# Kernel tuning notes

Measured on AMD Instinct MI355X. Metric: run time of the kernel, lower is better.

The kernel has to match this reference:

```python
import jax, jax.numpy as jnp
import numpy as np

WINDOW_SIZE = 11
SIGMA = 1.5
CHANNEL = 3
L = 2.0
C1 = (0.01 * L) ** 2
C2 = (0.03 * L) ** 2
WEIGHTS = jnp.asarray([0.0448, 0.2856, 0.3001, 0.2363, 0.1333], dtype=jnp.float32)


def _create_window(window_size=WINDOW_SIZE, channel=CHANNEL):
    x = jnp.arange(window_size, dtype=jnp.float32)
    g = jnp.exp(-((x - window_size // 2) ** 2) / (2.0 * SIGMA ** 2))
    g = g / g.sum()
    w2d = jnp.outer(g, g)  # (ws, ws)
    # depthwise kernel, OIHW with I=1, O=channel
    return jnp.broadcast_to(w2d[None, None], (channel, 1, window_size, window_size))


def _depthwise_conv(x, w):
    # x: (B,C,H,W), w: (C,1,kh,kw), groups=C, VALID padding
    return jax.lax.conv_general_dilated(
        x, w, window_strides=(1, 1), padding='VALID',
        feature_group_count=x.shape[1],
        dimension_numbers=('NCHW', 'OIHW', 'NCHW'))


def _ssim_level(img1, img2, window):
    mu1 = _depthwise_conv(img1, window)
    mu2 = _depthwise_conv(img2, window)
    mu1_sq = mu1 * mu1
    mu2_sq = mu2 * mu2
    mu1_mu2 = mu1 * mu2
    sigma1_sq = _depthwise_conv(img1 * img1, window) - mu1_sq
    sigma2_sq = _depthwise_conv(img2 * img2, window) - mu2_sq
    sigma12 = _depthwise_conv(img1 * img2, window) - mu1_mu2
    v1 = 2.0 * sigma12 + C2
    v2 = sigma1_sq + sigma2_sq + C2
    cs = jnp.mean(v1 / v2)
    ssim_map = (2.0 * mu1_mu2 + C1) * v1 / ((mu1_sq + mu2_sq + C1) * v2)
    return jnp.mean(ssim_map), cs


def _avg_pool2(x):
    b, c, h, w = x.shape
    return x.reshape(b, c, h // 2, 2, w // 2, 2).mean(axis=(3, 5))


def _msssim(img1, img2):
    window = _create_window()
    mssim, mcs = [], []
    for _ in range(WEIGHTS.shape[0]):
        sim, cs = _ssim_level(img1, img2, window)
        mssim.append(sim)
        mcs.append(cs)
        img1 = _avg_pool2(img1)
        img2 = _avg_pool2(img2)
    mssim = jnp.stack(mssim)
    mcs = jnp.stack(mcs)
    # normalize=True
    mssim = (mssim + 1.0) / 2.0
    mcs = (mcs + 1.0) / 2.0
    pow1 = mcs ** WEIGHTS
    pow2 = mssim ** WEIGHTS
    # faithful to source: prod over broadcast of pow1[:-1] * pow2[-1]
    return jnp.prod(pow1[:-1] * pow2[-1])


def setup_inputs() -> dict:
    key = jax.random.key(0)
    k1, k2 = jax.random.split(key)
    shape = (16, 3, 512, 512)
    output = jax.random.uniform(k1, shape, dtype=jnp.float32)
    gt = jax.random.uniform(k2, shape, dtype=jnp.float32)
    return {"output": output, "gt": gt}


def reference(output, gt):
    return 1.0 - _msssim(output, gt)
```

## Files before the change

kernel.cpp:

```cpp
#include <hip/hip_runtime.h>
#include <math.h>

typedef float vf2 __attribute__((ext_vector_type(2)));

__device__ __forceinline__ vf2 pk_fma(vf2 a, vf2 b, vf2 c) {
    vf2 d;
    asm("v_pk_fma_f32 %0, %1, %2, %3" : "=v"(d) : "v"(a), "v"(b), "v"(c));
    return d;
}
__device__ __forceinline__ vf2 pk_mul(vf2 a, vf2 b) {
    vf2 d;
    asm("v_pk_mul_f32 %0, %1, %2" : "=v"(d) : "v"(a), "v"(b));
    return d;
}
__device__ __forceinline__ vf2 pk_fma_blo(vf2 w, vf2 b, vf2 c) {
    vf2 d;
    asm("v_pk_fma_f32 %0, %1, %2, %3 op_sel_hi:[0,1,1]"
        : "=v"(d) : "v"(w), "v"(b), "v"(c));
    return d;
}
__device__ __forceinline__ vf2 pk_fma_bhi(vf2 w, vf2 b, vf2 c) {
    vf2 d;
    asm("v_pk_fma_f32 %0, %1, %2, %3 op_sel:[1,0,0] op_sel_hi:[1,1,1]"
        : "=v"(d) : "v"(w), "v"(b), "v"(c));
    return d;
}

#define L0_H 512
#define L0_HOUT 502
#define L0_HP 256
#define L0_SEG 64
#define L0_NCHUNK 7
#define ROWW 536
#define NQ 134
#define CARRY_BASE (11 * ROWW)
#define STREAM_WORDS (CARRY_BASE + 2 * ROWW)

__global__ __launch_bounds__(256)
void msssim_stream_l0(const float* __restrict__ img1,
                      const float* __restrict__ img2,
                      double* __restrict__ sums,
                      float* __restrict__ poolP, float* __restrict__ poolQ)
{
    __shared__ __align__(16) float buf[STREAM_WORDS];
    __shared__ float wred[4][2];

    const float gs[11] = {0.00102838f, 0.00759875f, 0.03600077f, 0.10936070f,
                          0.21300554f, 0.26601173f, 0.21300554f, 0.10936070f,
                          0.03600077f, 0.00759875f, 0.00102838f};

    const int tid = threadIdx.x;
    const int c0 = blockIdx.x * 256;
    const int oy0 = blockIdx.y * L0_SEG;
    const long long plane = (long long)blockIdx.z * L0_H * L0_H;
    const long long pplane = (long long)blockIdx.z * L0_HP * L0_HP;
    const bool colok = (c0 + tid) < L0_HOUT;

    const int par = tid & 1;
    vf2 wp[6];
    #pragma unroll
    for (int jq = 0; jq < 6; ++jq) {
        const int i0 = 2 * jq, i1 = 2 * jq + 1;
        const float we0 = (i0 < 11) ? gs[i0] : 0.f;
        const float wo0 = (i0 >= 1) ? gs[i0 - 1] : 0.f;
        const float we1 = (i1 < 11) ? gs[i1] : 0.f;
        const float wo1 = (i1 >= 1) ? gs[i1 - 1] : 0.f;
        wp[jq].x = par ? wo0 : we0;
        wp[jq].y = par ? wo1 : we1;
    }
    vf2 wgv[6];
    #pragma unroll
    for (int k = 0; k < 6; ++k) { wgv[k].x = gs[k]; wgv[k].y = gs[k]; }

    int rowS[6], colS[6], ldsoff[6], rHS[6];
    #pragma unroll
    for (int t = 0; t < 6; ++t) {
        const int s = tid + 256 * t;
        if (s < 11 * NQ) {
            const int r = s / NQ, q = s - NQ * r;
            rowS[t] = r;
            colS[t] = c0 + 2 * q;
            ldsoff[t] = r * ROWW + q * 4;
            rHS[t] = r * L0_H;
        } else { rowS[t] = -1; colS[t] = 0; ldsoff[t] = 0; rHS[t] = 0; }
    }

    float4 pf[6];
    auto prefetch = [&](int ybase) {
        const int yH = ybase * L0_H;
        #pragma unroll
        for (int t = 0; t < 6; ++t) {
            float2 a = make_float2(0.f, 0.f), b = make_float2(0.f, 0.f);
            if (rowS[t] >= 0) {
                const int y = ybase + rowS[t];
                if (y < L0_H && colS[t] < L0_H) {
                    const long long idx = plane + yH + rHS[t] + colS[t];
                    a = *(const float2*)(img1 + idx);
                    b = *(const float2*)(img2 + idx);
                }
            }
            pf[t] = make_float4(a.x + b.x, a.x - b.x, a.y + b.y, a.y - b.y);
        }
    };
    auto stage_write = [&]() {
        #pragma unroll
        for (int t = 0; t < 6; ++t)
            if (rowS[t] >= 0) *(float4*)&buf[ldsoff[t]] = pf[t];
    };

    prefetch(oy0);
    stage_write();
    __syncthreads();

    vf2 pd_pq[11], pd_sq[11];
    #pragma unroll
    for (int s = 0; s < 11; ++s) { pd_pq[s] = (vf2){0.f, 0.f}; pd_sq[s] = (vf2){0.f, 0.f}; }

    const int qb4 = (tid >> 1) * 4;
    const float C1 = 4.0e-4f, C2 = 3.6e-3f;
    float ssim_acc = 0.f, cs_acc = 0.f;

    for (int c = 0; c < L0_NCHUNK; ++c) {
        const int cs = oy0 + 11 * c;
        const bool more = (c + 1 < L0_NCHUNK);

        if (more) prefetch(cs + 11);

        if (tid < 128) {
            const int px = (c0 >> 1) + tid;
            const int t4 = tid * 4;
            for (int jp = (cs & 1); jp + 1 <= 10; jp += 2) {
                const int py = (cs + jp) >> 1;
                if (py < L0_HP) {
                    const float4 v0 = *(const float4*)&buf[jp * ROWW + t4];
                    const float4 v1 = *(const float4*)&buf[(jp + 1) * ROWW + t4];
                    poolP[pplane + py * L0_HP + px] = 0.25f * (v0.x + v0.z + v1.x + v1.z);
                    poolQ[pplane + py * L0_HP + px] = 0.25f * (v0.y + v0.w + v1.y + v1.w);
                }
            }
            if (c > 0 && (cs & 1)) {
                const int py = (cs - 1) >> 1;
                if (py < L0_HP) {
                    const float4 v0 = *(const float4*)&buf[CARRY_BASE + ((c - 1) & 1) * ROWW + t4];
                    const float4 v1 = *(const float4*)&buf[t4];
                    poolP[pplane + py * L0_HP + px] = 0.25f * (v0.x + v0.z + v1.x + v1.z);
                    poolQ[pplane + py * L0_HP + px] = 0.25f * (v0.y + v0.w + v1.y + v1.w);
                }
            }
        }
        if (((cs & 1) == 0) && more && tid < NQ) {
            *(float4*)&buf[CARRY_BASE + (c & 1) * ROWW + tid * 4] =
                *(const float4*)&buf[10 * ROWW + tid * 4];
        }

        #pragma unroll
        for (int j = 0; j < 11; ++j) {
            float4 q[6];
            const int rw = j * ROWW + qb4;
            #pragma unroll
            for (int u = 0; u < 6; ++u) q[u] = *(const float4*)&buf[rw + 4 * u];

            vf2 hpq = {0.f, 0.f}, hsq = {0.f, 0.f};
            #pragma unroll
            for (int u = 0; u < 6; ++u) {
                const vf2 elo = {q[u].x, q[u].y};
                const vf2 ehi = {q[u].z, q[u].w};
                const vf2 slo = pk_mul(elo, elo);
                const vf2 shi = pk_mul(ehi, ehi);
                hpq = pk_fma_blo(wp[u], elo, hpq);
                hpq = pk_fma_bhi(wp[u], ehi, hpq);
                hsq = pk_fma_blo(wp[u], slo, hsq);
                hsq = pk_fma_bhi(wp[u], shi, hsq);
            }
            #pragma unroll
            for (int k = 0; k < 11; ++k) {
                const int s = (j - k + 11) % 11;
                const int m = (k <= 5) ? k : 10 - k;
                pd_pq[s] = pk_fma(wgv[m], hpq, pd_pq[s]);
                pd_sq[s] = pk_fma(wgv[m], hsq, pd_sq[s]);
            }
            const int yrel = 11 * c + j;
            if (yrel >= 10) {
                const int s = (j + 1) % 11;
                const int orow = yrel - 10;
                if (orow < L0_SEG && (oy0 + orow) < L0_HOUT && colok) {
                    const vf2 musq = pk_mul(pd_pq[s], pd_pq[s]);
                    const float sP = pd_sq[s].x - musq.x;
                    const float sQ = pd_sq[s].y - musq.y;
                    const float v1 = 0.5f * (sP - sQ) + C2;
                    const float v2 = 0.5f * (sP + sQ) + C2;
                    const float num1 = 0.5f * (musq.x - musq.y) + C1;
                    const float den1 = 0.5f * (musq.x + musq.y) + C1;
                    cs_acc += v1 * __builtin_amdgcn_rcpf(v2);
                    ssim_acc += num1 * v1 * __builtin_amdgcn_rcpf(den1 * v2);
                }
                pd_pq[s] = (vf2){0.f, 0.f};
                pd_sq[s] = (vf2){0.f, 0.f};
            }
        }

        __syncthreads();
        if (more) stage_write();
        __syncthreads();
    }

    #pragma unroll
    for (int off = 32; off > 0; off >>= 1) {
        ssim_acc += __shfl_down(ssim_acc, off);
        cs_acc   += __shfl_down(cs_acc, off);
    }
    const int wave = tid >> 6;
    if ((tid & 63) == 0) { wred[wave][0] = ssim_acc; wred[wave][1] = cs_acc; }
    __syncthreads();
    if (tid == 0) {
        atomicAdd(&sums[0], (double)(wred[0][0] + wred[1][0] + wred[2][0] + wred[3][0]));
        atomicAdd(&sums[5], (double)(wred[0][1] + wred[1][1] + wred[2][1] + wred[3][1]));
    }
}

#define TILE 32
#define IN_DIM 42
#define SCP 21
#define HALO 10
#define STAGE_WORDS (IN_DIM * SCP * 4)
#define SH 340
#define HB STAGE_WORDS
#define SMEM_WORDS (HB + 16 * SH)

__global__ __launch_bounds__(256)
void msssim_level_kernel(const float* __restrict__ src1,
                         const float* __restrict__ src2,
                         int H, int level, int tiles_per_seg, int pq_input,
                         double* __restrict__ sums,
                         float* __restrict__ pool1, float* __restrict__ pool2)
{
    __shared__ __align__(16) float smem[SMEM_WORDS];
    __shared__ float wred[4][2];

    const float g[11] = {0.00102838f, 0.00759875f, 0.03600077f, 0.10936070f,
                         0.21300554f, 0.26601173f, 0.21300554f, 0.10936070f,
                         0.03600077f, 0.00759875f, 0.00102838f};
    vf2 wg[11];
    #pragma unroll
    for (int k = 0; k < 11; ++k) { wg[k].x = g[k]; wg[k].y = g[k]; }

    const int tid = threadIdx.x;
    const int Hout = H - HALO;
    const int ntiles = (Hout + TILE - 1) / TILE;
    const int tstart = blockIdx.y * tiles_per_seg;
    const int tend = min(ntiles, tstart + tiles_per_seg);
    const int ox0 = blockIdx.x * TILE;
    const int Hp = H >> 1;
    const long long base = (long long)blockIdx.z * H * H;

    int rHS[4], rS[4], xS[4];
    #pragma unroll
    for (int t4 = 0; t4 < 4; ++t4) {
        const int s = tid + 256 * t4;
        if (s < IN_DIM * SCP) {
            const int r = s / SCP, cp = s - r * SCP;
            rS[t4] = r; rHS[t4] = r * H; xS[t4] = ox0 + 2 * cp;
        } else { rS[t4] = -1; rHS[t4] = 0; xS[t4] = 0; }
    }

    auto load_slot = [&](int t4, int ybase) -> float4 {
        float2 a = make_float2(0.f, 0.f), b = make_float2(0.f, 0.f);
        if (rS[t4] >= 0) {
            const int y = ybase + rS[t4], x = xS[t4];
            if (y < H && x < H) {
                const long long idx = base + (long long)ybase * H + rHS[t4] + x;
                a = *(const float2*)(src1 + idx);
                b = *(const float2*)(src2 + idx);
            }
        }
        if (pq_input) return make_float4(a.x, b.x, a.y, b.y);
        return make_float4(a.x + b.x, a.x - b.x, a.y + b.y, a.y - b.y);
    };

    float4 pref[4];
    {
        #pragma unroll
        for (int t4 = 0; t4 < 4; ++t4) pref[t4] = load_slot(t4, tstart * TILE);
        #pragma unroll
        for (int t4 = 0; t4 < 4; ++t4)
            if (rS[t4] >= 0) *(float4*)&smem[(tid + 256 * t4) * 4] = pref[t4];
    }
    __syncthreads();

    float ssim_acc = 0.f, cs_acc = 0.f;

    for (int tt = tstart; tt < tend; ++tt) {
        const int ty0 = tt * TILE;
        const bool more = (tt + 1 < tend);

        if (more) {
            #pragma unroll
            for (int t4 = 0; t4 < 4; ++t4) pref[t4] = load_slot(t4, ty0 + TILE);
        }

        if (pool1 != nullptr) {
            const int pr = tid >> 4, pc = tid & 15;
            const int py = (ty0 >> 1) + pr, px = (ox0 >> 1) + pc;
            if (py < Hp && px < Hp) {
                const float4 v0 = *(const float4*)&smem[(2 * pr * SCP + pc) * 4];
                const float4 v1 = *(const float4*)&smem[((2 * pr + 1) * SCP + pc) * 4];
                const long long ob = (long long)blockIdx.z * Hp * Hp + (long long)py * Hp + px;
                pool1[ob] = 0.25f * (v0.x + v0.z + v1.x + v1.z);
                pool2[ob] = 0.25f * (v0.y + v0.w + v1.y + v1.w);
            }
        }

        float4 hA[3], hBv[3];
        #pragma unroll
        for (int t = 0; t < 3; ++t) {
            const int p = tid + 256 * t;
            if (p < IN_DIM * 16) {
                const int r = p >> 4, m = p & 15;
                vf2 Apq = {0.f, 0.f}, Asq = {0.f, 0.f};
                vf2 Bpq = {0.f, 0.f}, Bsq = {0.f, 0.f};
                #pragma unroll
                for (int jj = 0; jj < 6; ++jj) {
                    const float4 v = *(const float4*)&smem[(r * SCP + m + jj) * 4];
                    const vf2 lo = {v.x, v.y};
                    const vf2 hi = {v.z, v.w};
                    const vf2 losq = pk_mul(lo, lo);
                    const vf2 hisq = pk_mul(hi, hi);
                    Apq = pk_fma(wg[2 * jj], lo, Apq);
                    Asq = pk_fma(wg[2 * jj], losq, Asq);
                    if (jj >= 1) {
                        Bpq = pk_fma(wg[2 * jj - 1], lo, Bpq);
                        Bsq = pk_fma(wg[2 * jj - 1], losq, Bsq);
                    }
                    if (jj <= 4) {
                        Apq = pk_fma(wg[2 * jj + 1], hi, Apq);
                        Asq = pk_fma(wg[2 * jj + 1], hisq, Asq);
                    }
                    Bpq = pk_fma(wg[2 * jj], hi, Bpq);
                    Bsq = pk_fma(wg[2 * jj], hisq, Bsq);
                }
                hA[t]  = make_float4(Apq.x, Apq.y, Asq.x, Asq.y);
                hBv[t] = make_float4(Bpq.x, Bpq.y, Bsq.x, Bsq.y);
            }
        }
        __syncthreads();

        #pragma unroll
        for (int t = 0; t < 3; ++t) {
            const int p = tid + 256 * t;
            if (p < IN_DIM * 16) {
                const int r = p >> 4, m = p & 15;
                const int hb = HB + m * SH + r * 8;
                *(float4*)&smem[hb]     = hA[t];
                *(float4*)&smem[hb + 4] = hBv[t];
            }
        }
        if (more) {
            #pragma unroll
            for (int t4 = 0; t4 < 4; ++t4)
                if (rS[t4] >= 0) *(float4*)&smem[(tid + 256 * t4) * 4] = pref[t4];
        }
        __syncthreads();

        const int tx = tid & 31, rg = tid >> 5;
        const int r0 = rg * 4;
        const int m = tx >> 1, par = tx & 1;
        const int hb = HB + m * SH + par * 4;

        vf2 accPQ[4], accSQ[4];
        #pragma unroll
        for (int o = 0; o < 4; ++o) {
            accPQ[o] = (vf2){0.f, 0.f};
            accSQ[o] = (vf2){0.f, 0.f};
        }
        #pragma unroll
        for (int i = 0; i < 14; ++i) {
            const float4 h4 = *(const float4*)&smem[hb + (r0 + i) * 8];
            const vf2 ppq = {h4.x, h4.y};
            const vf2 psq = {h4.z, h4.w};
            #pragma unroll
            for (int o = 0; o < 4; ++o) {
                const int k = i - o;
                if (k >= 0 && k <= 10) {
                    accPQ[o] = pk_fma(wg[k], ppq, accPQ[o]);
                    accSQ[o] = pk_fma(wg[k], psq, accSQ[o]);
                }
            }
        }

        const float C1 = 4.0e-4f;
        const float C2 = 3.6e-3f;
        const int ox = ox0 + tx;
        #pragma unroll
        for (int o = 0; o < 4; ++o) {
            const int oy = ty0 + r0 + o;
            if (oy < Hout && ox < Hout) {
                const vf2 musq = pk_mul(accPQ[o], accPQ[o]);
                const float sP = accSQ[o].x - musq.x;
                const float sQ = accSQ[o].y - musq.y;
                const float v1 = 0.5f * (sP - sQ) + C2;
                const float v2 = 0.5f * (sP + sQ) + C2;
                const float num1 = 0.5f * (musq.x - musq.y) + C1;
                const float den1 = 0.5f * (musq.x + musq.y) + C1;
                cs_acc += v1 * __builtin_amdgcn_rcpf(v2);
                ssim_acc += num1 * v1 * __builtin_amdgcn_rcpf(den1 * v2);
            }
        }
    }

    #pragma unroll
    for (int off = 32; off > 0; off >>= 1) {
        ssim_acc += __shfl_down(ssim_acc, off);
        cs_acc   += __shfl_down(cs_acc, off);
    }
    const int wave = tid >> 6;
    if ((tid & 63) == 0) { wred[wave][0] = ssim_acc; wred[wave][1] = cs_acc; }
    __syncthreads();
    if (tid == 0) {
        const float s = wred[0][0] + wred[1][0] + wred[2][0] + wred[3][0];
        const float c = wred[0][1] + wred[1][1] + wred[2][1] + wred[3][1];
        atomicAdd(&sums[level],     (double)s);
        atomicAdd(&sums[5 + level], (double)c);
    }
}

__global__ void msssim_final_kernel(const double* __restrict__ sums,
                                    float* __restrict__ out)
{
    if (threadIdx.x == 0 && blockIdx.x == 0) {
        const double W[5] = {0.0448, 0.2856, 0.3001, 0.2363, 0.1333};
        const int Houts[5] = {502, 246, 118, 54, 22};
        double mssim[5], mcs[5];
        for (int l = 0; l < 5; ++l) {
            const double cnt = 48.0 * (double)Houts[l] * (double)Houts[l];
            mssim[l] = (sums[l]     / cnt + 1.0) * 0.5;
            mcs[l]   = (sums[5 + l] / cnt + 1.0) * 0.5;
        }
        const double p2 = pow(mssim[4], W[4]);
        double prod = 1.0;
        for (int l = 0; l < 4; ++l) prod *= pow(mcs[l], W[l]) * p2;
        out[0] = (float)(1.0 - prod);
    }
}

extern "C" void kernel_launch(void* const* d_in, const int* in_sizes, int n_in,
                              void* d_out, int out_size, void* d_ws, size_t ws_size,
                              hipStream_t stream)
{
    const float* img1 = (const float*)d_in[0];
    const float* img2 = (const float*)d_in[1];
    float* out = (float*)d_out;
    (void)in_sizes; (void)n_in; (void)out_size; (void)ws_size;

    char* ws = (char*)d_ws;
    double* sums = (double*)ws;
    float* X1 = (float*)(ws + 256);
    float* X2 = X1 + 3145728;
    float* Y1 = X2 + 3145728;
    float* Y2 = Y1 + 786432;

    hipMemsetAsync(sums, 0, 10 * sizeof(double), stream);

    hipLaunchKernelGGL(msssim_stream_l0, dim3(2, 8, 48), dim3(256), 0, stream,
                       img1, img2, sums, X1, X2);

    auto launch_level = [&](const float* a, const float* b, int H, int level,
                            int segs, float* pa, float* pb) {
        const int Hout = H - HALO;
        const int strips = (Hout + TILE - 1) / TILE;
        const int ntiles = (Hout + TILE - 1) / TILE;
        const int tps = (ntiles + segs - 1) / segs;
        dim3 grid(strips, segs, 48);
        hipLaunchKernelGGL(msssim_level_kernel, grid, dim3(256), 0, stream,
                           a, b, H, level, tps, 1, sums, pa, pb);
    };

    launch_level(X1, X2, 256, 1, 2, Y1, Y2);
    launch_level(Y1, Y2, 128, 2, 4, X1, X2);
    launch_level(X1, X2, 64, 3, 2, Y1, Y2);
    launch_level(Y1, Y2, 32, 4, 1, nullptr, nullptr);

    hipLaunchKernelGGL(msssim_final_kernel, dim3(1), dim3(64), 0, stream, sums, out);
}
```

Baseline: 143.5 us.

## Halve level-0 row segment and replace op_sel packed FMAs with pre-broadcast weights

Cuts the level-0 streaming kernel's row segment from 64 to 32 output rows and doubles the grid in y, so more blocks are in flight. The op_sel-based packed FMAs are replaced by plain packed FMAs that use weights broadcast into both lanes, which costs six extra weight registers. Shorter segments mean each block reloads the 10-row halo more often, adding redundant loads and horizontal-pass work in exchange for better occupancy and load balance.

```diff
diff --git a/kernel.cpp b/kernel.cpp
--- a/kernel.cpp
+++ b/kernel.cpp
@@ -13,24 +13,12 @@
     asm("v_pk_mul_f32 %0, %1, %2" : "=v"(d) : "v"(a), "v"(b));
     return d;
 }
-__device__ __forceinline__ vf2 pk_fma_blo(vf2 w, vf2 b, vf2 c) {
-    vf2 d;
-    asm("v_pk_fma_f32 %0, %1, %2, %3 op_sel_hi:[0,1,1]"
-        : "=v"(d) : "v"(w), "v"(b), "v"(c));
-    return d;
-}
-__device__ __forceinline__ vf2 pk_fma_bhi(vf2 w, vf2 b, vf2 c) {
-    vf2 d;
-    asm("v_pk_fma_f32 %0, %1, %2, %3 op_sel:[1,0,0] op_sel_hi:[1,1,1]"
-        : "=v"(d) : "v"(w), "v"(b), "v"(c));
-    return d;
-}
 
 #define L0_H 512
 #define L0_HOUT 502
 #define L0_HP 256
-#define L0_SEG 64
-#define L0_NCHUNK 7
+#define L0_SEG 32
+#define L0_NCHUNK 4
 #define ROWW 536
 #define NQ 134
 #define CARRY_BASE (11 * ROWW)
@@ -57,16 +45,17 @@
     const bool colok = (c0 + tid) < L0_HOUT;
 
     const int par = tid & 1;
-    vf2 wp[6];
-    #pragma unroll
-    for (int jq = 0; jq < 6; ++jq) {
-        const int i0 = 2 * jq, i1 = 2 * jq + 1;
-        const float we0 = (i0 < 11) ? gs[i0] : 0.f;
-        const float wo0 = (i0 >= 1) ? gs[i0 - 1] : 0.f;
-        const float we1 = (i1 < 11) ? gs[i1] : 0.f;
-        const float wo1 = (i1 >= 1) ? gs[i1 - 1] : 0.f;
-        wp[jq].x = par ? wo0 : we0;
-        wp[jq].y = par ? wo1 : we1;
+    vf2 wbl[6], wbh[6];
+    #pragma unroll
+    for (int u = 0; u < 6; ++u) {
+        const float we_lo = (2 * u < 11) ? gs[2 * u] : 0.f;
+        const float wo_lo = (2 * u >= 1) ? gs[2 * u - 1] : 0.f;
+        const float we_hi = (2 * u + 1 < 11) ? gs[2 * u + 1] : 0.f;
+        const float wo_hi = gs[2 * u];
+        const float wl = par ? wo_lo : we_lo;
+        const float wh = par ? wo_hi : we_hi;
+        wbl[u].x = wl; wbl[u].y = wl;
+        wbh[u].x = wh; wbh[u].y = wh;
     }
     vf2 wgv[6];
     #pragma unroll
@@ -167,10 +156,10 @@
                 const vf2 ehi = {q[u].z, q[u].w};
                 const vf2 slo = pk_mul(elo, elo);
                 const vf2 shi = pk_mul(ehi, ehi);
-                hpq = pk_fma_blo(wp[u], elo, hpq);
-                hpq = pk_fma_bhi(wp[u], ehi, hpq);
-                hsq = pk_fma_blo(wp[u], slo, hsq);
-                hsq = pk_fma_bhi(wp[u], shi, hsq);
+                hpq = pk_fma(wbl[u], elo, hpq);
+                hpq = pk_fma(wbh[u], ehi, hpq);
+                hsq = pk_fma(wbl[u], slo, hsq);
+                hsq = pk_fma(wbh[u], shi, hsq);
             }
             #pragma unroll
             for (int k = 0; k < 11; ++k) {
@@ -460,7 +449,7 @@
 
     hipMemsetAsync(sums, 0, 10 * sizeof(double), stream);
 
-    hipLaunchKernelGGL(msssim_stream_l0, dim3(2, 8, 48), dim3(256), 0, stream,
+    hipLaunchKernelGGL(msssim_stream_l0, dim3(2, 16, 48), dim3(256), 0, stream,
                        img1, img2, sums, X1, X2);
 
     auto launch_level = [&](const float* a, const float* b, int H, int level,
```

Measured after the change: 160.1 us. 1.12x slower.
